# Performance work log

Measured on AMD Instinct MI355X. Metric: run time of the kernel, lower is better.

Reference implementation:

```python
import jax, jax.numpy as jnp
import numpy as np

B, T, H = 2, 2048, 1024
I = 4096            # intermediate dim
HEADS = 4
RET = 128           # private expert retrieval dim
NUM_EXPERTS = 4096
NUM_KEYS = 64       # sqrt(NUM_EXPERTS)
K = 8               # num_cdmmoe_experts_per_head


def setup_inputs() -> dict:
    key = jax.random.key(0)
    ks = jax.random.split(key, 7)
    return {
        "hidden_states": jax.random.normal(ks[0], (B, T, H), jnp.float32),
        "W_up": jax.random.normal(ks[1], (I, H), jnp.float32) * 0.02,
        "W_down": jax.random.normal(ks[2], (H, I), jnp.float32) * 0.02,
        "W_q": jax.random.normal(ks[3], (HEADS * RET, H), jnp.float32) * 0.02,
        "keys": jax.random.normal(ks[4], (HEADS, NUM_KEYS, 2, RET // 2), jnp.float32) * 0.02,
        "down_embed": jax.random.normal(ks[5], (NUM_EXPERTS, H), jnp.float32) * 0.02,
        "up_embed": jax.random.normal(ks[6], (NUM_EXPERTS, H), jnp.float32) * 0.02,
    }


def reference(hidden_states, W_up, W_down, W_q, keys, down_embed, up_embed):
    b, t, hd = hidden_states.shape
    h, nk, _, n = keys.shape  # heads, num_keys, 2, half retrieval dim
    # queries: [b,t,h*2n] -> [2,b,t,h,n]
    q = jnp.einsum('btd,ed->bte', hidden_states, W_q)
    q = q.reshape(b, t, 2, h, n).transpose(2, 0, 1, 3, 4)
    # product-key similarities: [2,b,t,h,num_keys]
    sim = jnp.einsum('pbthn,hkpn->pbthk', q, keys)
    scores_xy, idx_xy = jax.lax.top_k(sim, K)  # [2,b,t,h,K]
    sx, sy = scores_xy[0], scores_xy[1]
    ix, iy = idx_xy[0], idx_xy[1]
    # cartesian combine: [b,t,h,K*K]
    all_scores = (sx[..., :, None] + sy[..., None, :]).reshape(b, t, h, K * K)
    all_idx = (ix[..., :, None] * nk + iy[..., None, :]).reshape(b, t, h, K * K)
    scores, pk = jax.lax.top_k(all_scores, K)               # [b,t,h,K]
    indices = jnp.take_along_axis(all_idx, pk, axis=-1)     # [b,t,h,K]
    de = down_embed[indices]  # [b,t,h,K,H]
    ue = up_embed[indices]    # [b,t,h,K,H]
    w = jax.nn.silu(jnp.einsum('btd,bthkd->bthk', hidden_states, de)
                    * jax.nn.softmax(scores, axis=-1))
    experts_states = jnp.einsum('bthk,bthkd->btd', w, ue)
    dense = jnp.einsum('bti,di->btd', jax.nn.silu(jnp.einsum('btd,id->bti', hidden_states, W_up)), W_down)
    return dense + experts_states
```

## Files before the change

kernel.cpp:

```cpp
#include <hip/hip_runtime.h>

typedef unsigned short u16;
typedef unsigned int u32;

#define TOKENS 4096
#define HDIM 1024
#define IDIM 4096
#define NHEADS 4
#define NKEYS 64
#define TOPK 8
#define QDIM 512

typedef __bf16 bf16x8 __attribute__((ext_vector_type(8)));
typedef float  f32x4  __attribute__((ext_vector_type(4)));
typedef u16    u16x8  __attribute__((ext_vector_type(8)));
typedef u32    u32x4  __attribute__((ext_vector_type(4)));

__device__ __forceinline__ u16 f2bf(float f) {
    u32 u = __float_as_uint(f);
    u += 0x7fffu + ((u >> 16) & 1u);
    return (u16)(u >> 16);
}
__device__ __forceinline__ float bf2f(u16 h) { return __uint_as_float(((u32)h) << 16); }

#define H_N4   1048576
#define WUP_N4 1048576
#define WDN_N4 1048576
#define DE_N4  1048576
#define UE_N4  1048576
#define CVT_TOT (H_N4 + WUP_N4 + WDN_N4 + DE_N4 + UE_N4)

__device__ __forceinline__ void cvt1(const float* in, u16* hi, u16* lo, int i) {
    float4 v = reinterpret_cast<const float4*>(in)[i];
    float vf[4] = {v.x, v.y, v.z, v.w};
    ushort4 h;
    u16 hh[4];
#pragma unroll
    for (int j = 0; j < 4; j++) hh[j] = f2bf(vf[j]);
    h.x = hh[0]; h.y = hh[1]; h.z = hh[2]; h.w = hh[3];
    reinterpret_cast<ushort4*>(hi)[i] = h;
    if (lo) {
        ushort4 l4;
        u16 ll[4];
#pragma unroll
        for (int j = 0; j < 4; j++) ll[j] = f2bf(vf[j] - bf2f(hh[j]));
        l4.x = ll[0]; l4.y = ll[1]; l4.z = ll[2]; l4.w = ll[3];
        reinterpret_cast<ushort4*>(lo)[i] = l4;
    }
}

__device__ __forceinline__ void cvt1_f8(const float* in, u32* out8, int i) {
    float4 v = reinterpret_cast<const float4*>(in)[i];
    u32 w = __builtin_amdgcn_cvt_pk_fp8_f32(v.x, v.y, 0u, false);
    w = __builtin_amdgcn_cvt_pk_fp8_f32(v.z, v.w, w, true);
    out8[i] = w;
}

__global__ __launch_bounds__(256) void cvt_all(
    const float* __restrict__ hidden, const float* __restrict__ W_up,
    const float* __restrict__ W_down, const float* __restrict__ de,
    const float* __restrict__ ue,
    u16* __restrict__ hid_hi, u16* __restrict__ hid_lo,
    u16* __restrict__ wup, u16* __restrict__ wdn,
    u32* __restrict__ de_f8, u32* __restrict__ ue_f8) {
    int i = blockIdx.x * 256 + threadIdx.x;
    if (i >= CVT_TOT) return;
    if (i < H_N4) { cvt1(hidden, hid_hi, hid_lo, i); return; }
    i -= H_N4;
    if (i < WUP_N4) { cvt1(W_up, wup, nullptr, i); return; }
    i -= WUP_N4;
    if (i < WDN_N4) { cvt1(W_down, wdn, nullptr, i); return; }
    i -= WDN_N4;
    if (i < DE_N4) { cvt1_f8(de, de_f8, i); return; }
    i -= DE_N4;
    cvt1_f8(ue, ue_f8, i);
}

__global__ __launch_bounds__(256) void weff_kernel(
    const float* __restrict__ keys, const float* __restrict__ Wq,
    u16* __restrict__ weff_hi, u16* __restrict__ weff_lo) {
    __shared__ float kk[64][65];
    __shared__ float wq_s[64][128];

    const int g = blockIdx.x >> 3, ds = blockIdx.x & 7;
    const int p = g >> 2, h = g & 3;
    const int d0 = ds * 128;
    const int t = threadIdx.x;
    const int base = p * 256 + h * 64;

    {
        int k = t >> 2, part = t & 3;
        const float* krow = keys + (((size_t)(h * NKEYS + k) * 2 + p) * 64);
#pragma unroll
        for (int j = 0; j < 4; j++) {
            int n0 = part * 16 + j * 4;
            float4 v = *reinterpret_cast<const float4*>(krow + n0);
            kk[k][n0 + 0] = v.x; kk[k][n0 + 1] = v.y;
            kk[k][n0 + 2] = v.z; kk[k][n0 + 3] = v.w;
        }
    }
    {
        int n = t >> 2, dpart = t & 3;
        const float* wrow = Wq + (size_t)(base + n) * HDIM + d0;
#pragma unroll
        for (int j = 0; j < 8; j++) {
            int dd = dpart * 32 + j * 4;
            float4 v = *reinterpret_cast<const float4*>(wrow + dd);
            *reinterpret_cast<float4*>(&wq_s[n][dd]) = v;
        }
    }
    __syncthreads();

    const int k = t & 63, dq = t >> 6;
    float acc[32];
#pragma unroll
    for (int i = 0; i < 32; i++) acc[i] = 0.f;
    for (int n = 0; n < 64; n++) {
        float kv = kk[k][n];
        const float4* wrow = reinterpret_cast<const float4*>(&wq_s[n][dq * 32]);
#pragma unroll
        for (int j = 0; j < 8; j++) {
            float4 w4 = wrow[j];
            acc[j * 4 + 0] += kv * w4.x; acc[j * 4 + 1] += kv * w4.y;
            acc[j * 4 + 2] += kv * w4.z; acc[j * 4 + 3] += kv * w4.w;
        }
    }
    size_t ro = (size_t)(g * 64 + k) * HDIM + d0 + dq * 32;
#pragma unroll
    for (int j = 0; j < 8; j++) {
        ushort4 hh, ll;
        u16 hv[4], lv[4];
#pragma unroll
        for (int i = 0; i < 4; i++) {
            float a = acc[j * 4 + i];
            hv[i] = f2bf(a);
            lv[i] = f2bf(a - bf2f(hv[i]));
        }
        hh.x = hv[0]; hh.y = hv[1]; hh.z = hv[2]; hh.w = hv[3];
        ll.x = lv[0]; ll.y = lv[1]; ll.z = lv[2]; ll.w = lv[3];
        *reinterpret_cast<ushort4*>(weff_hi + ro + j * 4) = hh;
        *reinterpret_cast<ushort4*>(weff_lo + ro + j * 4) = ll;
    }
}

__global__ __launch_bounds__(256) void reduce_add(float* __restrict__ out,
                                                  const float* __restrict__ p, int n4) {
    int i = blockIdx.x * 256 + threadIdx.x;
    if (i >= n4) return;
    float4 a = reinterpret_cast<const float4*>(out)[i];
    float4 b = reinterpret_cast<const float4*>(p)[i];
    a.x += b.x; a.y += b.y; a.z += b.z; a.w += b.w;
    reinterpret_cast<float4*>(out)[i] = a;
}

__device__ __forceinline__ void gload16(const void* g, void* s) {
    auto gp = reinterpret_cast<const __attribute__((address_space(1))) u32*>(
        reinterpret_cast<uintptr_t>(g));
    auto sp = reinterpret_cast<__attribute__((address_space(3))) u32*>(
        reinterpret_cast<uintptr_t>(s));
    __builtin_amdgcn_global_load_lds(gp, sp, 16, 0, 0);
}

#define BK 32

__device__ __forceinline__ int swz(int a) { return a ^ (((a >> 7) & 3) << 4); }

template <int ROWS, int THREADS>
__device__ __forceinline__ void stage_tile(const u16* g, size_t krow_b, size_t kb0,
                                           char* s, int t) {
#pragma unroll
    for (int rnd = 0; rnd < ROWS * 64 / (THREADS * 16); rnd++) {
        int o = t * 16 + rnd * THREADS * 16;
        int os = swz(o);
        int row = o >> 6, kb = os & 63;
        gload16((const char*)g + (size_t)row * krow_b + kb0 + kb, s + o);
    }
}

template <int N>
__device__ __forceinline__ void vm_wait() {
    if constexpr (N == 0) asm volatile("s_waitcnt vmcnt(0)" ::: "memory");
    else if constexpr (N == 3) asm volatile("s_waitcnt vmcnt(3)" ::: "memory");
    else if constexpr (N == 4) asm volatile("s_waitcnt vmcnt(4)" ::: "memory");
    else if constexpr (N == 6) asm volatile("s_waitcnt vmcnt(6)" ::: "memory");
    else if constexpr (N == 8) asm volatile("s_waitcnt vmcnt(8)" ::: "memory");
    else static_assert(N == 0, "unsupported vmcnt");
}

__device__ void up_body(char* smem, int bx, int by,
                        const u16* __restrict__ A, const u16* __restrict__ B,
                        u16* __restrict__ act, int M, int N, int K) {
    constexpr int LPS = 3;
    const int t = threadIdx.x;
    const int lane = t & 63;
    const int wave = t >> 6;
    const int wr = wave >> 1, wc = wave & 1;
    const int ro = lane & 15;
    const int ko = (lane >> 4) * 16;
    const int m0 = by * 256, n0 = bx * 128;

    f32x4 acc[4][4];
#pragma unroll
    for (int i = 0; i < 4; i++)
#pragma unroll
        for (int j = 0; j < 4; j++) acc[i][j] = (f32x4){0.f, 0.f, 0.f, 0.f};

    const size_t krow = (size_t)K * 2;
    const u16* Ab = A + (size_t)m0 * K;
    const u16* Bb = B + (size_t)n0 * K;
    char* smA = smem;
    char* smB = smem + 49152;

    auto stage_all = [&](int b, int k0) {
        size_t kb0 = (size_t)k0 * 2;
        stage_tile<256, 512>(Ab, krow, kb0, smA + b * 16384, t);
        stage_tile<128, 512>(Bb, krow, kb0, smB + b * 8192, t);
    };

    const int NU = K / BK;
    stage_all(0, 0);
    stage_all(1, BK);

    int cur = 0, pre = 2;
    for (int u = 0; u < NU; ++u) {
        if (u + 2 < NU) stage_all(pre, (u + 2) * BK);
        if (u + 2 < NU) vm_wait<2 * LPS>();
        else if (u + 1 < NU) vm_wait<LPS>();
        else vm_wait<0>();
        __builtin_amdgcn_s_barrier();

        const char* Ac = smA + cur * 16384;
        const char* Bc = smB + cur * 8192;
        bf16x8 fa[4], fb[4];
#pragma unroll
        for (int i = 0; i < 4; i++)
            fa[i] = *reinterpret_cast<const bf16x8*>(Ac + swz((wr * 64 + i * 16 + ro) * 64 + ko));
#pragma unroll
        for (int j = 0; j < 4; j++)
            fb[j] = *reinterpret_cast<const bf16x8*>(Bc + swz((wc * 64 + j * 16 + ro) * 64 + ko));
#pragma unroll
        for (int i = 0; i < 4; i++)
#pragma unroll
            for (int j = 0; j < 4; j++)
                acc[i][j] = __builtin_amdgcn_mfma_f32_16x16x32_bf16(fa[i], fb[j],
                                                                    acc[i][j], 0, 0, 0);
        __builtin_amdgcn_s_barrier();
        cur = (cur == 2) ? 0 : cur + 1;
        pre = (pre == 2) ? 0 : pre + 1;
    }

#pragma unroll
    for (int i = 0; i < 4; i++)
#pragma unroll
        for (int j = 0; j < 4; j++) {
            int col = n0 + wc * 64 + j * 16 + ro;
            int rbase = m0 + wr * 64 + i * 16 + (lane >> 4) * 4;
#pragma unroll
            for (int r = 0; r < 4; r++) {
                float v = acc[i][j][r];
                float s = v / (1.f + __expf(-v));
                act[(size_t)(rbase + r) * N + col] = f2bf(s);
            }
        }
}

__device__ void sim_body(char* smem, int bx, int by,
                         const u16* __restrict__ Ahi, const u16* __restrict__ Alo,
                         const u16* __restrict__ Bhi, const u16* __restrict__ Blo,
                         float* __restrict__ C, int M, int N, int K) {
    const int t = threadIdx.x;
    const int lane = t & 63;
    const int wave = t >> 6;
    const int wr = wave >> 2, wc = wave & 3;
    const int ro = lane & 15;
    const int ko = (lane >> 4) * 16;
    const int m0 = by * 64, n0 = bx * 128;

    f32x4 acc[2][2];
#pragma unroll
    for (int i = 0; i < 2; i++)
#pragma unroll
        for (int j = 0; j < 2; j++) acc[i][j] = (f32x4){0.f, 0.f, 0.f, 0.f};

    const size_t krow = (size_t)K * 2;
    const u16* Ahb = Ahi + (size_t)m0 * K;
    const u16* Alb = Alo + (size_t)m0 * K;
    const u16* Bhb = Bhi + (size_t)n0 * K;
    const u16* Blb = Blo + (size_t)n0 * K;
    char* smA = smem;
    char* smB = smem + 16384;

    auto stage_all = [&](int b, int k0) {
        size_t kb0 = (size_t)k0 * 2;
        {
            int sel = t >> 8, tt = t & 255;
            const u16* g = sel ? Alb : Ahb;
            int o = tt * 16;
            int os = swz(o);
            gload16((const char*)g + (size_t)(o >> 6) * krow + kb0 + (os & 63),
                    smA + b * 8192 + sel * 4096 + o);
        }
        {
            int o = t * 16, os = swz(o);
            gload16((const char*)Bhb + (size_t)(o >> 6) * krow + kb0 + (os & 63),
                    smB + b * 16384 + o);
        }
        {
            int o = t * 16, os = swz(o);
            gload16((const char*)Blb + (size_t)(o >> 6) * krow + kb0 + (os & 63),
                    smB + b * 16384 + 8192 + o);
        }
    };

    stage_all(0, 0);
    __syncthreads();
    int cur = 0;

    for (int k0 = 0; k0 < K; k0 += BK) {
        if (k0 + BK < K) stage_all(cur ^ 1, k0 + BK);
        const char* Ac = smA + cur * 8192;
        const char* Bc = smB + cur * 16384;
        bf16x8 fa[2], fal[2], fb[2], fbl[2];
#pragma unroll
        for (int i = 0; i < 2; i++) {
            int a = swz((wr * 32 + i * 16 + ro) * 64 + ko);
            fa[i] = *reinterpret_cast<const bf16x8*>(Ac + a);
            fal[i] = *reinterpret_cast<const bf16x8*>(Ac + 4096 + a);
        }
#pragma unroll
        for (int j = 0; j < 2; j++) {
            int a = swz((wc * 32 + j * 16 + ro) * 64 + ko);
            fb[j] = *reinterpret_cast<const bf16x8*>(Bc + a);
            fbl[j] = *reinterpret_cast<const bf16x8*>(Bc + 8192 + a);
        }
#pragma unroll
        for (int i = 0; i < 2; i++)
#pragma unroll
            for (int j = 0; j < 2; j++) {
                acc[i][j] = __builtin_amdgcn_mfma_f32_16x16x32_bf16(fa[i], fb[j],
                                                                    acc[i][j], 0, 0, 0);
                acc[i][j] = __builtin_amdgcn_mfma_f32_16x16x32_bf16(fa[i], fbl[j],
                                                                    acc[i][j], 0, 0, 0);
                acc[i][j] = __builtin_amdgcn_mfma_f32_16x16x32_bf16(fal[i], fb[j],
                                                                    acc[i][j], 0, 0, 0);
            }
        __syncthreads();
        cur ^= 1;
    }

#pragma unroll
    for (int i = 0; i < 2; i++)
#pragma unroll
        for (int j = 0; j < 2; j++) {
            int col = n0 + wc * 32 + j * 16 + ro;
            int rbase = m0 + wr * 32 + i * 16 + (lane >> 4) * 4;
#pragma unroll
            for (int r = 0; r < 4; r++)
                C[(size_t)(rbase + r) * N + col] = acc[i][j][r];
        }
}

__global__ __launch_bounds__(512, 4) void up_sim(
    const u16* __restrict__ hid_hi, const u16* __restrict__ hid_lo,
    const u16* __restrict__ wup,
    const u16* __restrict__ weff_hi, const u16* __restrict__ weff_lo,
    u16* __restrict__ act, float* __restrict__ Simb) {
    __shared__ char smem[73728];
    int bid = blockIdx.x;
    if (bid < 512) {
        int b2 = (bid & 7) * 64 + (bid >> 3);
        up_body(smem, b2 % 32, b2 / 32, hid_hi, wup, act, TOKENS, IDIM, HDIM);
    } else {
        int sb = bid - 512;
        sim_body(smem, sb & 3, sb >> 2, hid_hi, hid_lo, weff_hi, weff_lo, Simb,
                 TOKENS, QDIM, HDIM);
    }
}

template <int TBM, int TBN, int WVM, int WVN, int KCHUNKS>
__global__ __launch_bounds__(WVM * WVN * 64) void gemm_p3(
    const u16* __restrict__ A, const u16* __restrict__ B,
    void* __restrict__ Cout, void* __restrict__ Cout2,
    const float* __restrict__ ext, int M, int N, int K) {
    constexpr int THREADS = WVM * WVN * 64;
    constexpr int WM = TBM / WVM, WN = TBN / WVN;
    constexpr int FM = WM / 16, FN = WN / 16;
    constexpr int LPS = (TBM + TBN) * 64 / (THREADS * 16);
    __shared__ u16 As[3][TBM * BK];
    __shared__ u16 Bs[3][TBN * BK];
    const int t = threadIdx.x;
    const int lane = t & 63;
    const int wave = t >> 6;
    const int wr = wave / WVN, wc = wave % WVN;
    const int ro = lane & 15;
    const int ko = (lane >> 4) * 16;

    int bx = blockIdx.x, by = blockIdx.y;
    {
        int gx = gridDim.x;
        int n = gx * gridDim.y;
        int bid = by * gx + bx;
        int q = n >> 3;
        bid = (bid & 7) * q + (bid >> 3);
        bx = bid % gx; by = bid / gx;
    }
    const int m0 = by * TBM;
    const int n0 = bx * TBN;
    const int klen = K / KCHUNKS;
    const int z = (KCHUNKS > 1) ? blockIdx.z : 0;
    const int koff = z * klen;
    const int NU = klen / BK;

    f32x4 acc[FM][FN];
#pragma unroll
    for (int i = 0; i < FM; i++)
#pragma unroll
        for (int j = 0; j < FN; j++) acc[i][j] = (f32x4){0.f, 0.f, 0.f, 0.f};

    const size_t krow = (size_t)K * 2;
    const u16* Ab = A + (size_t)m0 * K;
    const u16* Bb = B + (size_t)n0 * K;

    auto stage_all = [&](int b, int k0) {
        size_t kb0 = (size_t)k0 * 2;
        stage_tile<TBM, THREADS>(Ab, krow, kb0, (char*)As[b], t);
        stage_tile<TBN, THREADS>(Bb, krow, kb0, (char*)Bs[b], t);
    };

    stage_all(0, koff);
    stage_all(1, koff + BK);

    int cur = 0, pre = 2;
    for (int u = 0; u < NU; ++u) {
        int k0 = koff + u * BK;
        if (u + 2 < NU) stage_all(pre, k0 + 2 * BK);
        if (u + 2 < NU) vm_wait<2 * LPS>();
        else if (u + 1 < NU) vm_wait<LPS>();
        else vm_wait<0>();
        __builtin_amdgcn_s_barrier();

        const u16* Ac = As[cur];
        const u16* Bc = Bs[cur];
        bf16x8 fa[FM], fb[FN];
#pragma unroll
        for (int i = 0; i < FM; i++)
            fa[i] = *reinterpret_cast<const bf16x8*>(
                (const char*)Ac + swz((wr * WM + i * 16 + ro) * 64 + ko));
#pragma unroll
        for (int j = 0; j < FN; j++)
            fb[j] = *reinterpret_cast<const bf16x8*>(
                (const char*)Bc + swz((wc * WN + j * 16 + ro) * 64 + ko));
#pragma unroll
        for (int i = 0; i < FM; i++)
#pragma unroll
            for (int j = 0; j < FN; j++)
                acc[i][j] = __builtin_amdgcn_mfma_f32_16x16x32_bf16(fa[i], fb[j],
                                                                    acc[i][j], 0, 0, 0);
        __builtin_amdgcn_s_barrier();
        cur = (cur == 2) ? 0 : cur + 1;
        pre = (pre == 2) ? 0 : pre + 1;
    }

#pragma unroll
    for (int i = 0; i < FM; i++)
#pragma unroll
        for (int j = 0; j < FN; j++) {
            int col = n0 + wc * WN + j * 16 + ro;
            int rbase = m0 + wr * WM + i * 16 + (lane >> 4) * 4;
#pragma unroll
            for (int r = 0; r < 4; r++) {
                float v = acc[i][j][r];
                size_t off = (size_t)(rbase + r) * N + col;
                if (KCHUNKS == 1 || z == 0)
                    ((float*)Cout)[off] = v + ext[off];
                else
                    ((float*)Cout2)[off] = v;
            }
        }
}

__device__ __forceinline__ int rank64(const float* base, float v, int l) {
    const float4* gv = reinterpret_cast<const float4*>(base);
    int rank = 0;
#pragma unroll
    for (int n = 0; n < 16; n++) {
        float4 o = gv[n];
        int b = n * 4;
        rank += (o.x > v) || (o.x == v && (b + 0) < l);
        rank += (o.y > v) || (o.y == v && (b + 1) < l);
        rank += (o.z > v) || (o.z == v && (b + 2) < l);
        rank += (o.w > v) || (o.w == v && (b + 3) < l);
    }
    return rank;
}

__global__ __launch_bounds__(512) void router_gather(
    const float* __restrict__ Simb, const u16* __restrict__ hid_bf,
    const u32* __restrict__ de_f8, const u32* __restrict__ ue_f8,
    float* __restrict__ expst) {
    __shared__ float sims[QDIM];
    __shared__ float topv[8][TOPK];
    __shared__ int topi[8][TOPK];
    __shared__ float pv[NHEADS][64];
    __shared__ float st8[NHEADS][TOPK];
    __shared__ int sid8[NHEADS][TOPK];
    __shared__ float gate8[NHEADS][TOPK];
    __shared__ float wks[NHEADS][TOPK];
    __shared__ float red[8][256];

    const int tok = blockIdx.x;
    const int tid = threadIdx.x;
    const int w = tid >> 6, l = tid & 63;

    sims[tid] = Simb[(size_t)tok * QDIM + tid];
    __syncthreads();

    {
        float v = sims[w * 64 + l];
        int rank = rank64(sims + w * 64, v, l);
        if (rank < TOPK) { topv[w][rank] = v; topi[w][rank] = l; }
    }
    __syncthreads();

    if (w < NHEADS) pv[w][l] = topv[w][l >> 3] + topv[4 + w][l & 7];
    __syncthreads();

    if (w < NHEADS) {
        float v = pv[w][l];
        int rank = rank64(pv[w], v, l);
        if (rank < TOPK) {
            st8[w][rank] = v;
            sid8[w][rank] = topi[w][l >> 3] * NKEYS + topi[4 + w][l & 7];
        }
    }
    __syncthreads();

    if (tid < NHEADS * TOPK) {
        int h = tid >> 3, r = tid & 7;
        float m0 = st8[h][0];
        float s = 0.f;
#pragma unroll
        for (int i = 0; i < TOPK; i++) s += __expf(st8[h][i] - m0);
        gate8[h][r] = __expf(st8[h][r] - m0) / s;
    }
    __syncthreads();

    {
        const int head = w >> 1, kq = (w & 1) * 4;
        u16x8 hv[2];
        const u16* hrow = hid_bf + (size_t)tok * HDIM + l * 16;
        hv[0] = *reinterpret_cast<const u16x8*>(hrow);
        hv[1] = *reinterpret_cast<const u16x8*>(hrow + 8);
        float h16[16];
#pragma unroll
        for (int t2 = 0; t2 < 8; t2++) {
            h16[t2] = bf2f(hv[0][t2]);
            h16[8 + t2] = bf2f(hv[1][t2]);
        }
        int eid[4];
        float gt[4];
#pragma unroll
        for (int j = 0; j < 4; j++) {
            eid[j] = sid8[head][kq + j];
            gt[j] = gate8[head][kq + j];
        }
        u32x4 dv[4];
#pragma unroll
        for (int j = 0; j < 4; j++)
            dv[j] = *reinterpret_cast<const u32x4*>(de_f8 + (size_t)eid[j] * 256 + l * 4);
        float dot[4];
#pragma unroll
        for (int j = 0; j < 4; j++) {
            float s = 0.f;
#pragma unroll
            for (int w2 = 0; w2 < 4; w2++) {
                u32 word = dv[j][w2];
                s += h16[w2 * 4 + 0] * __builtin_amdgcn_cvt_f32_fp8(word, 0);
                s += h16[w2 * 4 + 1] * __builtin_amdgcn_cvt_f32_fp8(word, 1);
                s += h16[w2 * 4 + 2] * __builtin_amdgcn_cvt_f32_fp8(word, 2);
                s += h16[w2 * 4 + 3] * __builtin_amdgcn_cvt_f32_fp8(word, 3);
            }
            dot[j] = s;
        }
#pragma unroll
        for (int m = 32; m; m >>= 1)
#pragma unroll
            for (int j = 0; j < 4; j++) dot[j] += __shfl_xor(dot[j], m, 64);
        if (l < 4) {
            float x = dot[l] * gt[l];
            wks[head][kq + l] = x / (1.f + __expf(-x));
        }
    }
    __syncthreads();

    {
        const int q = w >> 1, hf = w & 1;
        float acc0 = 0.f, acc1 = 0.f, acc2 = 0.f, acc3 = 0.f;
        const u32* ubase = ue_f8 + q * 64 + l;
#pragma unroll
        for (int m = 0; m < 16; m++) {
            int mm = hf * 16 + m;
            int h = mm >> 3, k = mm & 7;
            int e = sid8[h][k];
            float wk = wks[h][k];
            u32 u = ubase[(size_t)e * 256];
            acc0 += wk * __builtin_amdgcn_cvt_f32_fp8(u, 0);
            acc1 += wk * __builtin_amdgcn_cvt_f32_fp8(u, 1);
            acc2 += wk * __builtin_amdgcn_cvt_f32_fp8(u, 2);
            acc3 += wk * __builtin_amdgcn_cvt_f32_fp8(u, 3);
        }
        *reinterpret_cast<float4*>(&red[w][l * 4]) = make_float4(acc0, acc1, acc2, acc3);
    }
    __syncthreads();

    {
        int d = tid * 2;
        int qq = d >> 8, dq = d & 255;
        float2 a = *reinterpret_cast<float2*>(&red[2 * qq][dq]);
        float2 b = *reinterpret_cast<float2*>(&red[2 * qq + 1][dq]);
        float2 o;
        o.x = a.x + b.x;
        o.y = a.y + b.y;
        *reinterpret_cast<float2*>(expst + (size_t)tok * HDIM + d) = o;
    }
}

extern "C" void kernel_launch(void* const* d_in, const int* in_sizes, int n_in,
                              void* d_out, int out_size, void* d_ws, size_t ws_size,
                              hipStream_t stream) {
    const float* hidden = (const float*)d_in[0];
    const float* W_up = (const float*)d_in[1];
    const float* W_down = (const float*)d_in[2];
    const float* W_q = (const float*)d_in[3];
    const float* keys = (const float*)d_in[4];
    const float* down_embed = (const float*)d_in[5];
    const float* up_embed = (const float*)d_in[6];
    float* out = (float*)d_out;

    char* ws = (char*)d_ws;
    size_t off = 0;
    auto alloc = [&](size_t bytes) {
        void* p = ws + off;
        off += (bytes + 255) & ~(size_t)255;
        return p;
    };
    u16* hid_hi = (u16*)alloc((size_t)TOKENS * HDIM * 2);
    u16* hid_lo = (u16*)alloc((size_t)TOKENS * HDIM * 2);
    float* Simb = (float*)alloc((size_t)TOKENS * QDIM * 4);
    float* partial = (float*)hid_lo;
    u16* weff_hi = (u16*)alloc((size_t)QDIM * HDIM * 2);
    u16* weff_lo = (u16*)alloc((size_t)QDIM * HDIM * 2);
    u16* wup = (u16*)alloc((size_t)IDIM * HDIM * 2);
    u16* wdn = (u16*)alloc((size_t)HDIM * IDIM * 2);
    u16* act = (u16*)alloc((size_t)TOKENS * IDIM * 2);
    u32* de_f8 = (u32*)alloc((size_t)4096 * HDIM);
    u32* ue_f8 = (u32*)alloc((size_t)4096 * HDIM);
    float* expst = (float*)alloc((size_t)TOKENS * HDIM * 4);

    cvt_all<<<(CVT_TOT + 255) / 256, 256, 0, stream>>>(
        hidden, W_up, W_down, down_embed, up_embed,
        hid_hi, hid_lo, wup, wdn, de_f8, ue_f8);
    weff_kernel<<<64, 256, 0, stream>>>(keys, W_q, weff_hi, weff_lo);

    up_sim<<<768, 512, 0, stream>>>(hid_hi, hid_lo, wup, weff_hi, weff_lo, act, Simb);

    router_gather<<<TOKENS, 512, 0, stream>>>(Simb, hid_hi, de_f8, ue_f8, expst);

    gemm_p3<128, 128, 2, 2, 2>
        <<<dim3(HDIM / 128, TOKENS / 128, 2), 256, 0, stream>>>(
        act, wdn, out, partial, expst, TOKENS, HDIM, IDIM);
    reduce_add<<<(TOKENS * HDIM / 4 + 255) / 256, 256, 0, stream>>>(out, partial,
                                                                    TOKENS * HDIM / 4);
}
```

Before: 199.8 us.

## Overlap weight conversions with up/sim GEMM and split router across two blocks

The W_down bf16 conversion and the fp8 conversion of the expert embeddings move out of the initial conversion kernel into 256 extra blocks of the up_sim launch, so they run concurrently with the up and similarity GEMMs. router_gather now uses two 256-thread blocks per token, each handling half of the 32 selected experts and writing its own partial buffer, which removes the shared-memory reduction. The expert add also moves out of the GEMM epilogue into the final reduce kernel, which now sums four buffers. The cost is one extra full-size fp32 buffer and more global traffic in the reduce, and the top-k routing work is now done twice per token.

Measured after the change: 210.9 us. 1.06x slower.

```diff
diff --git a/kernel.cpp b/kernel.cpp
--- a/kernel.cpp
+++ b/kernel.cpp
@@ -28,7 +28,7 @@
 #define WDN_N4 1048576
 #define DE_N4  1048576
 #define UE_N4  1048576
-#define CVT_TOT (H_N4 + WUP_N4 + WDN_N4 + DE_N4 + UE_N4)
+#define CVT_TOT (H_N4 + WUP_N4)
 
 __device__ __forceinline__ void cvt1(const float* in, u16* hi, u16* lo, int i) {
     float4 v = reinterpret_cast<const float4*>(in)[i];
@@ -58,22 +58,12 @@
 
 __global__ __launch_bounds__(256) void cvt_all(
     const float* __restrict__ hidden, const float* __restrict__ W_up,
-    const float* __restrict__ W_down, const float* __restrict__ de,
-    const float* __restrict__ ue,
-    u16* __restrict__ hid_hi, u16* __restrict__ hid_lo,
-    u16* __restrict__ wup, u16* __restrict__ wdn,
-    u32* __restrict__ de_f8, u32* __restrict__ ue_f8) {
+    u16* __restrict__ hid_hi, u16* __restrict__ hid_lo, u16* __restrict__ wup) {
     int i = blockIdx.x * 256 + threadIdx.x;
     if (i >= CVT_TOT) return;
     if (i < H_N4) { cvt1(hidden, hid_hi, hid_lo, i); return; }
     i -= H_N4;
-    if (i < WUP_N4) { cvt1(W_up, wup, nullptr, i); return; }
-    i -= WUP_N4;
-    if (i < WDN_N4) { cvt1(W_down, wdn, nullptr, i); return; }
-    i -= WDN_N4;
-    if (i < DE_N4) { cvt1_f8(de, de_f8, i); return; }
-    i -= DE_N4;
-    cvt1_f8(ue, ue_f8, i);
+    cvt1(W_up, wup, nullptr, i);
 }
 
 __global__ __launch_bounds__(256) void weff_kernel(
@@ -143,13 +133,18 @@
     }
 }
 
-__global__ __launch_bounds__(256) void reduce_add(float* __restrict__ out,
-                                                  const float* __restrict__ p, int n4) {
+__global__ __launch_bounds__(256) void reduce_add4(float* __restrict__ out,
+                                                   const float* __restrict__ p,
+                                                   const float* __restrict__ ea,
+                                                   const float* __restrict__ eb, int n4) {
     int i = blockIdx.x * 256 + threadIdx.x;
     if (i >= n4) return;
     float4 a = reinterpret_cast<const float4*>(out)[i];
     float4 b = reinterpret_cast<const float4*>(p)[i];
-    a.x += b.x; a.y += b.y; a.z += b.z; a.w += b.w;
+    float4 c = reinterpret_cast<const float4*>(ea)[i];
+    float4 d = reinterpret_cast<const float4*>(eb)[i];
+    a.x += b.x + c.x + d.x; a.y += b.y + c.y + d.y;
+    a.z += b.z + c.z + d.z; a.w += b.w + c.w + d.w;
     reinterpret_cast<float4*>(out)[i] = a;
 }
 
@@ -364,24 +359,35 @@
     const u16* __restrict__ hid_hi, const u16* __restrict__ hid_lo,
     const u16* __restrict__ wup,
     const u16* __restrict__ weff_hi, const u16* __restrict__ weff_lo,
-    u16* __restrict__ act, float* __restrict__ Simb) {
+    const float* __restrict__ W_down, const float* __restrict__ de,
+    const float* __restrict__ ue,
+    u16* __restrict__ act, float* __restrict__ Simb,
+    u16* __restrict__ wdn, u32* __restrict__ de_f8, u32* __restrict__ ue_f8) {
     __shared__ char smem[73728];
     int bid = blockIdx.x;
     if (bid < 512) {
         int b2 = (bid & 7) * 64 + (bid >> 3);
         up_body(smem, b2 % 32, b2 / 32, hid_hi, wup, act, TOKENS, IDIM, HDIM);
-    } else {
+    } else if (bid < 768) {
         int sb = bid - 512;
         sim_body(smem, sb & 3, sb >> 2, hid_hi, hid_lo, weff_hi, weff_lo, Simb,
                  TOKENS, QDIM, HDIM);
+    } else {
+        int idx = (bid - 768) * 512 + threadIdx.x;
+#pragma unroll
+        for (int j = 0; j < 24; j++) {
+            int i = idx + j * 131072;
+            if (i < WDN_N4) cvt1(W_down, wdn, nullptr, i);
+            else if (i < WDN_N4 + DE_N4) cvt1_f8(de, de_f8, i - WDN_N4);
+            else cvt1_f8(ue, ue_f8, i - WDN_N4 - DE_N4);
+        }
     }
 }
 
 template <int TBM, int TBN, int WVM, int WVN, int KCHUNKS>
 __global__ __launch_bounds__(WVM * WVN * 64) void gemm_p3(
     const u16* __restrict__ A, const u16* __restrict__ B,
-    void* __restrict__ Cout, void* __restrict__ Cout2,
-    const float* __restrict__ ext, int M, int N, int K) {
+    float* __restrict__ Cout, float* __restrict__ Cout2, int M, int N, int K) {
     constexpr int THREADS = WVM * WVN * 64;
     constexpr int WM = TBM / WVM, WN = TBN / WVN;
     constexpr int FM = WM / 16, FN = WN / 16;
@@ -469,12 +475,9 @@
             int rbase = m0 + wr * WM + i * 16 + (lane >> 4) * 4;
 #pragma unroll
             for (int r = 0; r < 4; r++) {
-                float v = acc[i][j][r];
                 size_t off = (size_t)(rbase + r) * N + col;
-                if (KCHUNKS == 1 || z == 0)
-                    ((float*)Cout)[off] = v + ext[off];
-                else
-                    ((float*)Cout2)[off] = v;
+                if (z == 0) Cout[off] = acc[i][j][r];
+                else Cout2[off] = acc[i][j][r];
             }
         }
 }
@@ -494,10 +497,10 @@
     return rank;
 }
 
-__global__ __launch_bounds__(512) void router_gather(
+__global__ __launch_bounds__(256) void router_gather(
     const float* __restrict__ Simb, const u16* __restrict__ hid_bf,
     const u32* __restrict__ de_f8, const u32* __restrict__ ue_f8,
-    float* __restrict__ expst) {
+    float* __restrict__ expst_a, float* __restrict__ expst_b) {
     __shared__ float sims[QDIM];
     __shared__ float topv[8][TOPK];
     __shared__ int topi[8][TOPK];
@@ -505,27 +508,33 @@
     __shared__ float st8[NHEADS][TOPK];
     __shared__ int sid8[NHEADS][TOPK];
     __shared__ float gate8[NHEADS][TOPK];
-    __shared__ float wks[NHEADS][TOPK];
-    __shared__ float red[8][256];
-
-    const int tok = blockIdx.x;
+    __shared__ float wks_s[16];
+    __shared__ int eids_s[16];
+
+    const int tok = blockIdx.x >> 1;
+    const int hf2 = blockIdx.x & 1;
     const int tid = threadIdx.x;
     const int w = tid >> 6, l = tid & 63;
 
     sims[tid] = Simb[(size_t)tok * QDIM + tid];
+    sims[tid + 256] = Simb[(size_t)tok * QDIM + tid + 256];
     __syncthreads();
 
     {
-        float v = sims[w * 64 + l];
-        int rank = rank64(sims + w * 64, v, l);
-        if (rank < TOPK) { topv[w][rank] = v; topi[w][rank] = l; }
-    }
-    __syncthreads();
-
-    if (w < NHEADS) pv[w][l] = topv[w][l >> 3] + topv[4 + w][l & 7];
-    __syncthreads();
-
-    if (w < NHEADS) {
+#pragma unroll
+        for (int rep = 0; rep < 2; rep++) {
+            int g = w + rep * 4;
+            float v = sims[g * 64 + l];
+            int rank = rank64(sims + g * 64, v, l);
+            if (rank < TOPK) { topv[g][rank] = v; topi[g][rank] = l; }
+        }
+    }
+    __syncthreads();
+
+    pv[w][l] = topv[w][l >> 3] + topv[4 + w][l & 7];
+    __syncthreads();
+
+    {
         float v = pv[w][l];
         int rank = rank64(pv[w], v, l);
         if (rank < TOPK) {
@@ -546,7 +555,6 @@
     __syncthreads();
 
     {
-        const int head = w >> 1, kq = (w & 1) * 4;
         u16x8 hv[2];
         const u16* hrow = hid_bf + (size_t)tok * HDIM + l * 16;
         hv[0] = *reinterpret_cast<const u16x8*>(hrow);
@@ -561,8 +569,10 @@
         float gt[4];
 #pragma unroll
         for (int j = 0; j < 4; j++) {
-            eid[j] = sid8[head][kq + j];
-            gt[j] = gate8[head][kq + j];
+            int i32 = hf2 * 16 + w * 4 + j;
+            int h = i32 >> 3, k = i32 & 7;
+            eid[j] = sid8[h][k];
+            gt[j] = gate8[h][k];
         }
         u32x4 dv[4];
 #pragma unroll
@@ -588,40 +598,28 @@
             for (int j = 0; j < 4; j++) dot[j] += __shfl_xor(dot[j], m, 64);
         if (l < 4) {
             float x = dot[l] * gt[l];
-            wks[head][kq + l] = x / (1.f + __expf(-x));
+            wks_s[w * 4 + l] = x / (1.f + __expf(-x));
+            eids_s[w * 4 + l] = eid[l];
         }
     }
     __syncthreads();
 
     {
-        const int q = w >> 1, hf = w & 1;
         float acc0 = 0.f, acc1 = 0.f, acc2 = 0.f, acc3 = 0.f;
-        const u32* ubase = ue_f8 + q * 64 + l;
+        const u32* ubase = ue_f8 + w * 64 + l;
 #pragma unroll
         for (int m = 0; m < 16; m++) {
-            int mm = hf * 16 + m;
-            int h = mm >> 3, k = mm & 7;
-            int e = sid8[h][k];
-            float wk = wks[h][k];
+            int e = eids_s[m];
+            float wk = wks_s[m];
             u32 u = ubase[(size_t)e * 256];
             acc0 += wk * __builtin_amdgcn_cvt_f32_fp8(u, 0);
             acc1 += wk * __builtin_amdgcn_cvt_f32_fp8(u, 1);
             acc2 += wk * __builtin_amdgcn_cvt_f32_fp8(u, 2);
             acc3 += wk * __builtin_amdgcn_cvt_f32_fp8(u, 3);
         }
-        *reinterpret_cast<float4*>(&red[w][l * 4]) = make_float4(acc0, acc1, acc2, acc3);
-    }
-    __syncthreads();
-
-    {
-        int d = tid * 2;
-        int qq = d >> 8, dq = d & 255;
-        float2 a = *reinterpret_cast<float2*>(&red[2 * qq][dq]);
-        float2 b = *reinterpret_cast<float2*>(&red[2 * qq + 1][dq]);
-        float2 o;
-        o.x = a.x + b.x;
-        o.y = a.y + b.y;
-        *reinterpret_cast<float2*>(expst + (size_t)tok * HDIM + d) = o;
+        float* dst = (hf2 == 0) ? expst_a : expst_b;
+        *reinterpret_cast<float4*>(dst + (size_t)tok * HDIM + w * 256 + l * 4) =
+            make_float4(acc0, acc1, acc2, acc3);
     }
 }
 
@@ -655,20 +653,22 @@
     u16* act = (u16*)alloc((size_t)TOKENS * IDIM * 2);
     u32* de_f8 = (u32*)alloc((size_t)4096 * HDIM);
     u32* ue_f8 = (u32*)alloc((size_t)4096 * HDIM);
-    float* expst = (float*)alloc((size_t)TOKENS * HDIM * 4);
-
-    cvt_all<<<(CVT_TOT + 255) / 256, 256, 0, stream>>>(
-        hidden, W_up, W_down, down_embed, up_embed,
-        hid_hi, hid_lo, wup, wdn, de_f8, ue_f8);
+    float* expst_a = (float*)alloc((size_t)TOKENS * HDIM * 4);
+    float* expst_b = (float*)alloc((size_t)TOKENS * HDIM * 4);
+
+    cvt_all<<<(CVT_TOT + 255) / 256, 256, 0, stream>>>(hidden, W_up, hid_hi, hid_lo, wup);
     weff_kernel<<<64, 256, 0, stream>>>(keys, W_q, weff_hi, weff_lo);
 
-    up_sim<<<768, 512, 0, stream>>>(hid_hi, hid_lo, wup, weff_hi, weff_lo, act, Simb);
-
-    router_gather<<<TOKENS, 512, 0, stream>>>(Simb, hid_hi, de_f8, ue_f8, expst);
+    up_sim<<<1024, 512, 0, stream>>>(hid_hi, hid_lo, wup, weff_hi, weff_lo,
+                                     W_down, down_embed, up_embed,
+                                     act, Simb, wdn, de_f8, ue_f8);
+
+    router_gather<<<TOKENS * 2, 256, 0, stream>>>(Simb, hid_hi, de_f8, ue_f8,
+                                                  expst_a, expst_b);
 
     gemm_p3<128, 128, 2, 2, 2>
         <<<dim3(HDIM / 128, TOKENS / 128, 2), 256, 0, stream>>>(
-        act, wdn, out, partial, expst, TOKENS, HDIM, IDIM);
-    reduce_add<<<(TOKENS * HDIM / 4 + 255) / 256, 256, 0, stream>>>(out, partial,
-                                                                    TOKENS * HDIM / 4);
-}
+        act, wdn, out, partial, TOKENS, HDIM, IDIM);
+    reduce_add4<<<(TOKENS * HDIM / 4 + 255) / 256, 256, 0, stream>>>(
+        out, partial, expst_a, expst_b, TOKENS * HDIM / 4);
+}
```
